# Kernel tuning notes

Hardware: AMD Instinct MI355X
Metric: run time of the kernel (lower is better)

Reference implementation:

```python
import jax, jax.numpy as jnp
import numpy as np

Q_HEADS, KV_HEADS, DIMS = 16, 4, 1024
HEAD_DIM = DIMS // Q_HEADS          # 64
GROUPS = Q_HEADS // KV_HEADS        # 4


def rope(x):
    # x: [..., s, d]; base-10 thetas, positions start at 1 (per source RoPE)
    s, d = x.shape[-2], x.shape[-1]
    thetas = 10.0 ** (-jnp.arange(d // 2, dtype=jnp.float32))
    angles = jnp.arange(1, s + 1, dtype=jnp.float32)[:, None] * thetas  # [s, d/2]
    cos, sin = jnp.cos(angles), jnp.sin(angles)
    xr, xi = x[..., ::2], x[..., 1::2]
    outr = xr * cos - xi * sin
    outi = xr * sin + xi * cos
    return jnp.stack([outr, outi], axis=-1).reshape(x.shape)  # re-interleave


def setup_inputs() -> dict:
    key = jax.random.key(0)
    ks = jax.random.split(key, 5)
    b, s, in_dim = 4, 2048, 1024
    q = jax.random.normal(ks[0], (b, s, in_dim), dtype=jnp.float32)
    mask = jnp.tril(jnp.ones((s, s), dtype=jnp.float32))  # 1 = keep, 0 = masked
    sc = 1.0 / np.sqrt(in_dim)
    Wq = jax.random.normal(ks[1], (in_dim, Q_HEADS, HEAD_DIM), dtype=jnp.float32) * sc
    Wk = jax.random.normal(ks[2], (in_dim, KV_HEADS, HEAD_DIM), dtype=jnp.float32) * sc
    Wv = jax.random.normal(ks[3], (in_dim, KV_HEADS, HEAD_DIM), dtype=jnp.float32) * sc
    Wo = jax.random.normal(ks[4], (KV_HEADS * HEAD_DIM, in_dim), dtype=jnp.float32) * (1.0 / np.sqrt(KV_HEADS * HEAD_DIM))
    return {"q": q, "mask": mask, "Wq": Wq, "Wk": Wk, "Wv": Wv, "Wo": Wo}


def reference(q, mask, Wq, Wk, Wv, Wo):
    b, s, in_dim = q.shape
    # projections (DenseGeneral, no bias)
    qh = jnp.einsum('bsi,ihd->bshd', q, Wq)   # [b, s, 16, 64]
    kh = jnp.einsum('bsi,ihd->bshd', q, Wk)   # [b, s, 4, 64]  (kv = q)
    vh = jnp.einsum('bsi,ihd->bshd', q, Wv)
    # '... s (h g) d -> ... g h s d' with g=GROUPS
    qh = qh.reshape(b, s, KV_HEADS, GROUPS, HEAD_DIM).transpose(0, 3, 2, 1, 4)  # [b,g,h,s,d]
    kh = kh.transpose(0, 2, 1, 3)  # [b, h, s, d]
    vh = vh.transpose(0, 2, 1, 3)
    qh = rope(qh)
    kh = rope(kh)
    # NOTE: source einsum sums over group axis g
    scores = jnp.einsum('bghsd,bhad->bhsa', qh, kh)  # [b, h, s, s]
    scores = scores - (1.0 / mask - 1.0)             # mask==0 -> -inf
    attn = jax.nn.softmax(scores / jnp.float32(HEAD_DIM ** 0.5), axis=-1)
    out = jnp.einsum('bhsa,bhad->bhsd', attn, vh)    # [b, h, s, d]
    out = out.transpose(0, 2, 1, 3).reshape(b, s, KV_HEADS * HEAD_DIM)
    return out @ Wo  # [b, s, in_dim]
```

## Files before the change

kernel.cpp:

```cpp
#include <hip/hip_runtime.h>
#include <math.h>

#define BATCH 4
#define SEQ   2048
#define DIN   1024
#define KVH   4
#define HD    64
#define MTOT  (BATCH*SEQ)
#define NPROJ 768
#define PROJ_STRIDE (BATCH*KVH*SEQ*HD)
#define NCHUNK_TOT 80

typedef unsigned short ushort_t;
typedef __attribute__((ext_vector_type(8))) short short8;
typedef __attribute__((ext_vector_type(4))) float f32x4;

#define QSCALE (0.125f * 1.44269504088896340736f)

__device__ inline ushort_t f2bf(float x) {
    union { float f; unsigned int u; } v; v.f = x;
    unsigned int r = v.u + 0x7fffu + ((v.u >> 16) & 1u);
    return (ushort_t)(r >> 16);
}
__device__ inline ushort_t f2bf_trunc(float x) {
    return (ushort_t)(__float_as_uint(x) >> 16);
}

__device__ inline void load16_lds(const ushort_t* g, ushort_t* l) {
    __builtin_amdgcn_global_load_lds(
        (const __attribute__((address_space(1))) void*)g,
        (__attribute__((address_space(3))) void*)l, 16, 0, 0);
}

__global__ __launch_bounds__(256) void pack_weights_kernel(
        const float* __restrict__ Wq, const float* __restrict__ Wk,
        const float* __restrict__ Wv, const float* __restrict__ Wo,
        ushort_t* __restrict__ Wcat_t, ushort_t* __restrict__ Wo_t) {
    int idx = blockIdx.x * 256 + threadIdx.x;
    if (idx < NPROJ * DIN) {
        int n = idx >> 10, k = idx & 1023;
        float v;
        if (n < 256) {
            const float* p = Wq + (size_t)k * 1024 + (n >> 6) * 256 + (n & 63);
            v = p[0] + p[64] + p[128] + p[192];
        } else if (n < 512) {
            v = Wk[(size_t)k * 256 + (n - 256)];
        } else {
            v = Wv[(size_t)k * 256 + (n - 512)];
        }
        Wcat_t[idx] = f2bf(v);
    } else {
        int t = idx - NPROJ * DIN;
        int n = t >> 8, k = t & 255;
        Wo_t[t] = f2bf(Wo[(size_t)k * 1024 + n]);
    }
}

__global__ __launch_bounds__(256) void convtobf_kernel(
        const float* __restrict__ X, ushort_t* __restrict__ Y) {
    int i = (blockIdx.x * 256 + threadIdx.x) * 4;
    float4 v = *(const float4*)&X[i];
    ushort4 o;
    o.x = f2bf(v.x); o.y = f2bf(v.y); o.z = f2bf(v.z); o.w = f2bf(v.w);
    *(ushort4*)&Y[i] = o;
}

template<int OUT_MODE>
__global__ __launch_bounds__(256) void gemm_mfma_kernel(
        const ushort_t* __restrict__ A, const ushort_t* __restrict__ Bt,
        float* __restrict__ Y, ushort_t* __restrict__ Vt, int K, int N) {
    __shared__ __align__(16) ushort_t As[128 * 32];
    __shared__ __align__(16) ushort_t Bs[128 * 32];
    const int tid  = threadIdx.x;
    const int w    = tid >> 6, lane = tid & 63;
    const int m15  = lane & 15, quad = lane >> 4;
    const int wm   = (w >> 1) * 64, wn = (w & 1) * 64;
    const int m0   = blockIdx.y * 128, n0 = blockIdx.x * 128;
    const int lr   = lane >> 2;
    const int lc   = (lane & 3) * 8;

    f32x4 acc[4][4];
    #pragma unroll
    for (int i = 0; i < 4; ++i)
        #pragma unroll
        for (int j = 0; j < 4; ++j) acc[i][j] = (f32x4){0.f, 0.f, 0.f, 0.f};

    for (int k0 = 0; k0 < K; k0 += 32) {
        __syncthreads();
        #pragma unroll
        for (int p = 0; p < 2; ++p) {
            int r = w * 32 + p * 16 + lr;
            load16_lds(A  + (size_t)(m0 + r) * K + k0 + lc, As + w * 1024 + p * 512);
            load16_lds(Bt + (size_t)(n0 + r) * K + k0 + lc, Bs + w * 1024 + p * 512);
        }
        __syncthreads();

        short8 af[4], bfm[4];
        #pragma unroll
        for (int i = 0; i < 4; ++i)
            af[i] = *(const short8*)&As[(wm + i * 16 + m15) * 32 + quad * 8];
        #pragma unroll
        for (int j = 0; j < 4; ++j)
            bfm[j] = *(const short8*)&Bs[(wn + j * 16 + m15) * 32 + quad * 8];
        #pragma unroll
        for (int i = 0; i < 4; ++i)
            #pragma unroll
            for (int j = 0; j < 4; ++j)
                acc[i][j] = __builtin_amdgcn_mfma_f32_16x16x32_bf16(
                                af[i], bfm[j], acc[i][j], 0, 0, 0);
    }

    if (OUT_MODE == 0) {
        #pragma unroll
        for (int i = 0; i < 4; ++i)
            #pragma unroll
            for (int r = 0; r < 4; ++r) {
                size_t row = (size_t)(m0 + wm + i * 16 + quad * 4 + r);
                #pragma unroll
                for (int j = 0; j < 4; ++j)
                    Y[row * N + n0 + wn + j * 16 + m15] = acc[i][j][r];
            }
    } else {
        #pragma unroll
        for (int j = 0; j < 4; ++j) {
            int c = n0 + wn + j * 16 + m15;
            int proj = c >> 8, cc = c & 255;
            int hd = cc >> 6, d = cc & 63;
            if (proj < 2) {
                float* Yp = Y + (size_t)proj * PROJ_STRIDE + (size_t)hd * SEQ * HD + d;
                #pragma unroll
                for (int i = 0; i < 4; ++i)
                    #pragma unroll
                    for (int r = 0; r < 4; ++r) {
                        int m = m0 + wm + i * 16 + quad * 4 + r;
                        int b = m >> 11, s = m & (SEQ - 1);
                        Yp[(((size_t)b * KVH) * SEQ + s) * HD] = acc[i][j][r];
                    }
            } else {
                ushort_t* Vp = Vt + (((size_t)hd * HD) + d) * SEQ;
                #pragma unroll
                for (int i = 0; i < 4; ++i)
                    #pragma unroll
                    for (int r = 0; r < 4; ++r) {
                        int m = m0 + wm + i * 16 + quad * 4 + r;
                        int b = m >> 11, s = m & (SEQ - 1);
                        Vp[(size_t)b * KVH * HD * SEQ + s] = f2bf(acc[i][j][r]);
                    }
            }
        }
    }
}

__global__ __launch_bounds__(256) void rope_convert_kernel(
        const float* __restrict__ Qe, const float* __restrict__ Kf,
        ushort_t* __restrict__ Qbf, ushort_t* __restrict__ Kbf) {
    int t = blockIdx.x * 256 + threadIdx.x;
    int j  = t & 31;
    int s  = (t >> 5) & (SEQ - 1);
    int bh = (t >> 16) & 15;
    int tz = t >> 20;
    size_t off = ((size_t)bh * SEQ + s) * HD + 2 * j;
    const float* src = (tz ? Kf : Qe) + off;
    float2 x = *(const float2*)src;
    float theta = exp10f(-(float)j);
    float ang = (float)(s + 1) * theta;
    float sn, cs;
    sincosf(ang, &sn, &cs);
    float outr = x.x * cs - x.y * sn;
    float outi = x.x * sn + x.y * cs;
    if (!tz) { outr *= QSCALE; outi *= QSCALE; }
    ushort_t* dst = (tz ? Kbf : Qbf) + off;
    dst[0] = f2bf(outr);
    dst[1] = f2bf(outi);
}

__global__ __launch_bounds__(256) void attn_mfma_kernel(
        const ushort_t* __restrict__ Qbf, const ushort_t* __restrict__ Kbf,
        const ushort_t* __restrict__ Vtbf, float* __restrict__ pO,
        float* __restrict__ pL) {
    __shared__ __align__(16) ushort_t Ks[64][72];
    __shared__ __align__(16) ushort_t Vts[64][72];
    __shared__ __align__(16) ushort_t Ps[4][16][72];
    const int tid  = threadIdx.x;
    const int w    = tid >> 6, lane = tid & 63;
    const int m15  = lane & 15, quad = lane >> 4;
    const int bh   = blockIdx.y;
    const int f    = blockIdx.x;
    int qt, ch;
    if (f < 8)       { qt = f;                  ch = 0; }
    else if (f < 24) { qt = 8  + ((f - 8) >> 1);  ch = (f - 8) & 1; }
    else if (f < 48) { qt = 16 + (f - 24) / 3;    ch = (f - 24) % 3; }
    else             { qt = 24 + ((f - 48) >> 2); ch = (f - 48) & 3; }
    const int q0 = qt * 64;
    const int kt_beg = ch * 8;
    const int kt_end = min(kt_beg + 8, qt + 1);

    const ushort_t* Qb  = Qbf  + (size_t)bh * SEQ * HD;
    const ushort_t* Kb  = Kbf  + (size_t)bh * SEQ * HD;
    const ushort_t* Vtb = Vtbf + (size_t)bh * HD * SEQ;

    const int qrow = q0 + w * 16 + m15;
    short8 qf0 = *(const short8*)(Qb + (size_t)qrow * HD + quad * 8);
    short8 qf1 = *(const short8*)(Qb + (size_t)qrow * HD + 32 + quad * 8);

    f32x4 o[4];
    #pragma unroll
    for (int nt = 0; nt < 4; ++nt) o[nt] = (f32x4){0.f, 0.f, 0.f, 0.f};
    float lacc[4] = {0.f, 0.f, 0.f, 0.f};

    const int sc_ = tid & 7;
    const int sr_ = tid >> 3;

    for (int kt = kt_beg; kt < kt_end; ++kt) {
        const int k0 = kt * 64;
        __syncthreads();
        #pragma unroll
        for (int p = 0; p < 2; ++p) {
            int r = sr_ + p * 32;
            *(short8*)&Ks[r][sc_*8]  = *(const short8*)(Kb  + (size_t)(k0 + r) * HD + sc_ * 8);
            *(short8*)&Vts[r][sc_*8] = *(const short8*)(Vtb + (size_t)r * SEQ + k0 + sc_ * 8);
        }
        __syncthreads();

        f32x4 sc4[4];
        #pragma unroll
        for (int nt = 0; nt < 4; ++nt) {
            f32x4 c = {0.f, 0.f, 0.f, 0.f};
            c = __builtin_amdgcn_mfma_f32_16x16x32_bf16(
                    qf0, *(const short8*)&Ks[nt*16 + m15][quad*8], c, 0, 0, 0);
            c = __builtin_amdgcn_mfma_f32_16x16x32_bf16(
                    qf1, *(const short8*)&Ks[nt*16 + m15][32 + quad*8], c, 0, 0, 0);
            sc4[nt] = c;
        }
        if (kt == qt) {
            #pragma unroll
            for (int nt = 0; nt < 4; ++nt) {
                int colg = k0 + nt*16 + m15;
                #pragma unroll
                for (int r = 0; r < 4; ++r) {
                    int rowg = q0 + w*16 + quad*4 + r;
                    if (colg > rowg) sc4[nt][r] = -INFINITY;
                }
            }
        }

        #pragma unroll
        for (int nt = 0; nt < 4; ++nt)
            #pragma unroll
            for (int r = 0; r < 4; ++r) {
                float e = exp2f(sc4[nt][r]);
                lacc[r] += e;
                Ps[w][quad*4 + r][nt*16 + m15] = f2bf_trunc(e);
            }

        short8 pa0 = *(const short8*)&Ps[w][m15][quad*8];
        short8 pa1 = *(const short8*)&Ps[w][m15][32 + quad*8];
        #pragma unroll
        for (int nt = 0; nt < 4; ++nt) {
            o[nt] = __builtin_amdgcn_mfma_f32_16x16x32_bf16(
                        pa0, *(const short8*)&Vts[nt*16 + m15][quad*8], o[nt], 0, 0, 0);
            o[nt] = __builtin_amdgcn_mfma_f32_16x16x32_bf16(
                        pa1, *(const short8*)&Vts[nt*16 + m15][32 + quad*8], o[nt], 0, 0, 0);
        }
    }

    const int blk = bh * NCHUNK_TOT + f;
    #pragma unroll
    for (int r = 0; r < 4; ++r) {
        float ls = lacc[r];
        ls += __shfl_xor(ls, 1);
        ls += __shfl_xor(ls, 2);
        ls += __shfl_xor(ls, 4);
        ls += __shfl_xor(ls, 8);
        int row = w * 16 + quad * 4 + r;
        if (m15 == 0) pL[(size_t)blk * 64 + row] = ls;
        #pragma unroll
        for (int nt = 0; nt < 4; ++nt)
            pO[(size_t)blk * 4096 + row * 64 + nt * 16 + m15] = o[nt][r];
    }
}

__device__ inline int flat_of(int qt, int ch) {
    if (qt < 8)  return qt;
    if (qt < 16) return 8 + (qt - 8) * 2 + ch;
    if (qt < 24) return 24 + (qt - 16) * 3 + ch;
    return 48 + (qt - 24) * 4 + ch;
}

__global__ __launch_bounds__(256) void combine_kernel(
        const float* __restrict__ pO, const float* __restrict__ pL,
        ushort_t* __restrict__ Out) {
    const int qt = blockIdx.x, bh = blockIdx.y;
    const int tid = threadIdx.x;
    const int row = tid >> 2;
    const int cb = (tid & 3) * 16;
    const int nch = (qt >> 3) + 1;
    float acc[16] = {};
    float lsum = 0.f;
    for (int c = 0; c < nch; ++c) {
        int blk = bh * NCHUNK_TOT + flat_of(qt, c);
        const float* po = pO + (size_t)blk * 4096 + row * 64 + cb;
        lsum += pL[(size_t)blk * 64 + row];
        #pragma unroll
        for (int j = 0; j < 4; ++j) {
            float4 v = *(const float4*)&po[j * 4];
            acc[j*4+0] += v.x; acc[j*4+1] += v.y;
            acc[j*4+2] += v.z; acc[j*4+3] += v.w;
        }
    }
    float inv = 1.0f / lsum;
    int b = bh >> 2, h = bh & 3;
    int s = qt * 64 + row;
    ushort_t tmp[16];
    #pragma unroll
    for (int j = 0; j < 16; ++j) tmp[j] = f2bf(acc[j] * inv);
    ushort_t* dst = Out + ((size_t)b * SEQ + s) * (KVH * HD) + h * HD + cb;
    *(uint4*)dst = ((uint4*)tmp)[0];
    *(uint4*)(dst + 8) = ((uint4*)tmp)[1];
}

extern "C" void kernel_launch(void* const* d_in, const int* in_sizes, int n_in,
                              void* d_out, int out_size, void* d_ws, size_t ws_size,
                              hipStream_t stream) {
    const float* q  = (const float*)d_in[0];
    const float* Wq = (const float*)d_in[2];
    const float* Wk = (const float*)d_in[3];
    const float* Wv = (const float*)d_in[4];
    const float* Wo = (const float*)d_in[5];
    float* out = (float*)d_out;

    char* base = (char*)d_ws;
    ushort_t* wcat_t  = (ushort_t*)(base);
    ushort_t* wo_t    = (ushort_t*)(base + 0x180000);
    ushort_t* qin_bf  = (ushort_t*)(base + 0x200000);
    ushort_t* attn_bf = (ushort_t*)(base + 0x200000);
    float*    pO      = (float*)(base + 0x600000);
    float*    q_eff   = (float*)(base + 0x1200000);
    float*    pL      = (float*)(base + 0x1A00000);
    ushort_t* q_bf    = (ushort_t*)(base + 0x2200000);
    ushort_t* k_bf    = (ushort_t*)(base + 0x2600000);
    ushort_t* vt_bf   = (ushort_t*)(base + 0x2A00000);

    pack_weights_kernel<<<(NPROJ * DIN + DIN * 256) / 256, 256, 0, stream>>>(
        Wq, Wk, Wv, Wo, wcat_t, wo_t);

    convtobf_kernel<<<(MTOT * DIN) / 1024, 256, 0, stream>>>(q, qin_bf);

    dim3 gproj(NPROJ / 128, MTOT / 128);
    gemm_mfma_kernel<1><<<gproj, 256, 0, stream>>>(qin_bf, wcat_t, q_eff, vt_bf,
                                                   DIN, NPROJ);

    rope_convert_kernel<<<(2 * 16 * SEQ * 32) / 256, 256, 0, stream>>>(
        q_eff, q_eff + PROJ_STRIDE, q_bf, k_bf);

    dim3 gattn(NCHUNK_TOT, BATCH * KVH);
    attn_mfma_kernel<<<gattn, 256, 0, stream>>>(q_bf, k_bf, vt_bf, pO, pL);

    dim3 gcomb(SEQ / 64, BATCH * KVH);
    combine_kernel<<<gcomb, 256, 0, stream>>>(pO, pL, attn_bf);

    dim3 gout(DIN / 128, MTOT / 128);
    gemm_mfma_kernel<0><<<gout, 256, 0, stream>>>(attn_bf, wo_t, out, nullptr,
                                                  KVH * HD, DIN);
}
```

Before: 205.6 us.

## Fuse RoPE into projection GEMM epilogue, prefetch K/V tiles, reverse attention block order

RoPE and the bf16 conversion now run inside the projection GEMM's epilogue. The rotation partner element comes from a lane shuffle, and the cos/sin values come from a precomputed table. This drops the fp32 Q/K round trip and the separate rope kernel. The attention kernel also prefetches the next K/V tile into registers while the current tile is staged, and it launches the heaviest query chunks first for better tail balance. The costs are an extra small table kernel, more epilogue work, and extra register pressure.

```diff
diff --git a/kernel.cpp b/kernel.cpp
--- a/kernel.cpp
+++ b/kernel.cpp
@@ -56,6 +56,15 @@
     }
 }
 
+__global__ __launch_bounds__(256) void ctab_kernel(float2* __restrict__ ctab) {
+    int t = blockIdx.x * 256 + threadIdx.x;
+    int j = t & 31, s = t >> 5;
+    float ang = (float)(s + 1) * exp10f(-(float)j);
+    float sn, cs;
+    sincosf(ang, &sn, &cs);
+    ctab[t] = make_float2(cs, sn);
+}
+
 __global__ __launch_bounds__(256) void convtobf_kernel(
         const float* __restrict__ X, ushort_t* __restrict__ Y) {
     int i = (blockIdx.x * 256 + threadIdx.x) * 4;
@@ -68,7 +77,9 @@
 template<int OUT_MODE>
 __global__ __launch_bounds__(256) void gemm_mfma_kernel(
         const ushort_t* __restrict__ A, const ushort_t* __restrict__ Bt,
-        float* __restrict__ Y, ushort_t* __restrict__ Vt, int K, int N) {
+        float* __restrict__ Y, ushort_t* __restrict__ Qbf,
+        ushort_t* __restrict__ Kbf, ushort_t* __restrict__ Vt,
+        const float2* __restrict__ ctab, int K, int N) {
     __shared__ __align__(16) ushort_t As[128 * 32];
     __shared__ __align__(16) ushort_t Bs[128 * 32];
     const int tid  = threadIdx.x;
@@ -127,14 +138,21 @@
             int proj = c >> 8, cc = c & 255;
             int hd = cc >> 6, d = cc & 63;
             if (proj < 2) {
-                float* Yp = Y + (size_t)proj * PROJ_STRIDE + (size_t)hd * SEQ * HD + d;
+                int jj = d >> 1;
+                float sgn = (d & 1) ? 1.0f : -1.0f;
+                float qs  = (proj == 0) ? QSCALE : 1.0f;
+                ushort_t* dst = (proj ? Kbf : Qbf) + (size_t)hd * SEQ * HD + d;
                 #pragma unroll
                 for (int i = 0; i < 4; ++i)
                     #pragma unroll
                     for (int r = 0; r < 4; ++r) {
                         int m = m0 + wm + i * 16 + quad * 4 + r;
                         int b = m >> 11, s = m & (SEQ - 1);
-                        Yp[(((size_t)b * KVH) * SEQ + s) * HD] = acc[i][j][r];
+                        float x = acc[i][j][r];
+                        float p = __shfl_xor(x, 1);
+                        float2 ct = ctab[s * 32 + jj];
+                        float o = (x * ct.x + sgn * p * ct.y) * qs;
+                        dst[(((size_t)b * KVH) * SEQ + s) * HD] = f2bf(o);
                     }
             } else {
                 ushort_t* Vp = Vt + (((size_t)hd * HD) + d) * SEQ;
@@ -151,29 +169,6 @@
     }
 }
 
-__global__ __launch_bounds__(256) void rope_convert_kernel(
-        const float* __restrict__ Qe, const float* __restrict__ Kf,
-        ushort_t* __restrict__ Qbf, ushort_t* __restrict__ Kbf) {
-    int t = blockIdx.x * 256 + threadIdx.x;
-    int j  = t & 31;
-    int s  = (t >> 5) & (SEQ - 1);
-    int bh = (t >> 16) & 15;
-    int tz = t >> 20;
-    size_t off = ((size_t)bh * SEQ + s) * HD + 2 * j;
-    const float* src = (tz ? Kf : Qe) + off;
-    float2 x = *(const float2*)src;
-    float theta = exp10f(-(float)j);
-    float ang = (float)(s + 1) * theta;
-    float sn, cs;
-    sincosf(ang, &sn, &cs);
-    float outr = x.x * cs - x.y * sn;
-    float outi = x.x * sn + x.y * cs;
-    if (!tz) { outr *= QSCALE; outi *= QSCALE; }
-    ushort_t* dst = (tz ? Kbf : Qbf) + off;
-    dst[0] = f2bf(outr);
-    dst[1] = f2bf(outi);
-}
-
 __global__ __launch_bounds__(256) void attn_mfma_kernel(
         const ushort_t* __restrict__ Qbf, const ushort_t* __restrict__ Kbf,
         const ushort_t* __restrict__ Vtbf, float* __restrict__ pO,
@@ -185,9 +180,9 @@
     const int w    = tid >> 6, lane = tid & 63;
     const int m15  = lane & 15, quad = lane >> 4;
     const int bh   = blockIdx.y;
-    const int f    = blockIdx.x;
+    const int f    = 79 - blockIdx.x;
     int qt, ch;
-    if (f < 8)       { qt = f;                  ch = 0; }
+    if (f < 8)       { qt = f;                    ch = 0; }
     else if (f < 24) { qt = 8  + ((f - 8) >> 1);  ch = (f - 8) & 1; }
     else if (f < 48) { qt = 16 + (f - 24) / 3;    ch = (f - 24) % 3; }
     else             { qt = 24 + ((f - 48) >> 2); ch = (f - 48) & 3; }
@@ -211,14 +206,28 @@
     const int sc_ = tid & 7;
     const int sr_ = tid >> 3;
 
+    short8 pk0, pk1, pv0, pv1;
+    {
+        const int k0 = kt_beg * 64;
+        pk0 = *(const short8*)(Kb  + (size_t)(k0 + sr_) * HD + sc_ * 8);
+        pk1 = *(const short8*)(Kb  + (size_t)(k0 + sr_ + 32) * HD + sc_ * 8);
+        pv0 = *(const short8*)(Vtb + (size_t)sr_ * SEQ + k0 + sc_ * 8);
+        pv1 = *(const short8*)(Vtb + (size_t)(sr_ + 32) * SEQ + k0 + sc_ * 8);
+    }
+
     for (int kt = kt_beg; kt < kt_end; ++kt) {
         const int k0 = kt * 64;
         __syncthreads();
-        #pragma unroll
-        for (int p = 0; p < 2; ++p) {
-            int r = sr_ + p * 32;
-            *(short8*)&Ks[r][sc_*8]  = *(const short8*)(Kb  + (size_t)(k0 + r) * HD + sc_ * 8);
-            *(short8*)&Vts[r][sc_*8] = *(const short8*)(Vtb + (size_t)r * SEQ + k0 + sc_ * 8);
+        *(short8*)&Ks[sr_][sc_*8]       = pk0;
+        *(short8*)&Ks[sr_ + 32][sc_*8]  = pk1;
+        *(short8*)&Vts[sr_][sc_*8]      = pv0;
+        *(short8*)&Vts[sr_ + 32][sc_*8] = pv1;
+        if (kt + 1 < kt_end) {
+            const int kn = k0 + 64;
+            pk0 = *(const short8*)(Kb  + (size_t)(kn + sr_) * HD + sc_ * 8);
+            pk1 = *(const short8*)(Kb  + (size_t)(kn + sr_ + 32) * HD + sc_ * 8);
+            pv0 = *(const short8*)(Vtb + (size_t)sr_ * SEQ + kn + sc_ * 8);
+            pv1 = *(const short8*)(Vtb + (size_t)(sr_ + 32) * SEQ + kn + sc_ * 8);
         }
         __syncthreads();
 
@@ -332,26 +341,25 @@
     char* base = (char*)d_ws;
     ushort_t* wcat_t  = (ushort_t*)(base);
     ushort_t* wo_t    = (ushort_t*)(base + 0x180000);
-    ushort_t* qin_bf  = (ushort_t*)(base + 0x200000);
-    ushort_t* attn_bf = (ushort_t*)(base + 0x200000);
-    float*    pO      = (float*)(base + 0x600000);
-    float*    q_eff   = (float*)(base + 0x1200000);
-    float*    pL      = (float*)(base + 0x1A00000);
-    ushort_t* q_bf    = (ushort_t*)(base + 0x2200000);
-    ushort_t* k_bf    = (ushort_t*)(base + 0x2600000);
-    ushort_t* vt_bf   = (ushort_t*)(base + 0x2A00000);
+    float2*   ctab    = (float2*)(base + 0x200000);
+    ushort_t* qin_bf  = (ushort_t*)(base + 0x280000);
+    ushort_t* attn_bf = (ushort_t*)(base + 0x280000);
+    float*    pO      = (float*)(base + 0x680000);
+    float*    pL      = (float*)(base + 0x1A80000);
+    ushort_t* q_bf    = (ushort_t*)(base + 0x1B00000);
+    ushort_t* k_bf    = (ushort_t*)(base + 0x1F00000);
+    ushort_t* vt_bf   = (ushort_t*)(base + 0x2300000);
 
     pack_weights_kernel<<<(NPROJ * DIN + DIN * 256) / 256, 256, 0, stream>>>(
         Wq, Wk, Wv, Wo, wcat_t, wo_t);
 
+    ctab_kernel<<<(SEQ * 32) / 256, 256, 0, stream>>>(ctab);
+
     convtobf_kernel<<<(MTOT * DIN) / 1024, 256, 0, stream>>>(q, qin_bf);
 
     dim3 gproj(NPROJ / 128, MTOT / 128);
-    gemm_mfma_kernel<1><<<gproj, 256, 0, stream>>>(qin_bf, wcat_t, q_eff, vt_bf,
-                                                   DIN, NPROJ);
-
-    rope_convert_kernel<<<(2 * 16 * SEQ * 32) / 256, 256, 0, stream>>>(
-        q_eff, q_eff + PROJ_STRIDE, q_bf, k_bf);
+    gemm_mfma_kernel<1><<<gproj, 256, 0, stream>>>(
+        qin_bf, wcat_t, nullptr, q_bf, k_bf, vt_bf, ctab, DIN, NPROJ);
 
     dim3 gattn(NCHUNK_TOT, BATCH * KVH);
     attn_mfma_kernel<<<gattn, 256, 0, stream>>>(q_bf, k_bf, vt_bf, pO, pL);
@@ -360,6 +368,6 @@
     combine_kernel<<<gcomb, 256, 0, stream>>>(pO, pL, attn_bf);
 
     dim3 gout(DIN / 128, MTOT / 128);
-    gemm_mfma_kernel<0><<<gout, 256, 0, stream>>>(attn_bf, wo_t, out, nullptr,
-                                                  KVH * HD, DIN);
-}
+    gemm_mfma_kernel<0><<<gout, 256, 0, stream>>>(
+        attn_bf, wo_t, out, nullptr, nullptr, nullptr, nullptr, KVH * HD, DIN);
+}
```

Measured after the change: 196.3 us. 1.05x faster.
